# Performance work log

Measured on AMD Instinct MI355X. Metric: run time of the kernel, lower is better.

The kernel has to match this reference:

```python
import jax, jax.numpy as jnp
import numpy as np

B, S, D, E = 4, 2048, 1024, 8
HD = D // E          # per-expert head dim = 128
ROPE = HD // 2       # rotary dims = 64 (32 complex pairs)


def setup_inputs() -> dict:
    key = jax.random.key(0)
    ks = jax.random.split(key, 5)
    x = jax.random.normal(ks[0], (B, S, D), dtype=jnp.float32)
    Wg = jax.random.normal(ks[1], (D, E), dtype=jnp.float32) * 0.02
    Wqkv = jax.random.normal(ks[2], (E, D, 3 * HD), dtype=jnp.float32) * 0.02
    Wff = jax.random.normal(ks[3], (E, HD, D), dtype=jnp.float32) * 0.02
    b_ff = jnp.zeros((D,), dtype=jnp.float32)
    # precompute_freqs_cis(qk_rope_head_dim=ROPE, seqlen=S), theta=10000
    inv = 1.0 / (10000.0 ** (np.arange(0, ROPE, 2, dtype=np.float32) / ROPE))  # [ROPE//2]
    ang = np.arange(S, dtype=np.float32)[:, None] * inv[None, :]               # [S, ROPE//2]
    cos = jnp.asarray(np.cos(ang), dtype=jnp.float32)
    sin = jnp.asarray(np.sin(ang), dtype=jnp.float32)
    return {"x": x, "Wg": Wg, "Wqkv": Wqkv, "Wff": Wff, "b_ff": b_ff, "cos": cos, "sin": sin}


def _apply_rope(x, cos, sin):
    # x: [B,S,E,HD]; rotate the second half (x_pe), keep first half (x_nope), cat (pe, nope)
    b, s, e, hd = x.shape
    x_nope, x_pe = x[..., : hd // 2], x[..., hd // 2 :]
    xr = x_pe.reshape(b, s, e, hd // 4, 2)
    re, im = xr[..., 0], xr[..., 1]
    c = cos[None, :, None, :]
    sn = sin[None, :, None, :]
    rot = jnp.stack([re * c - im * sn, re * sn + im * c], axis=-1).reshape(b, s, e, hd // 2)
    return jnp.concatenate([rot, x_nope], axis=-1)


def reference(x, Wg, Wqkv, Wff, b_ff, cos, sin):
    b, s, d = x.shape
    e, hd = Wqkv.shape[0], Wqkv.shape[2] // 3
    # RoPE on per-expert chunks
    xh = _apply_rope(x.reshape(b, s, e, hd), cos, sin).reshape(b, s, d)
    # SwitchGate: top-1 routing
    probs = jax.nn.softmax(xh @ Wg, axis=-1)            # [b,s,E]
    expert = jnp.argmax(probs, axis=-1)                 # [b,s]
    gate = jnp.max(probs, axis=-1)                      # [b,s]
    # preprocess: per-expert stable gather of routed tokens (capacity = s, padded+masked)
    is_e = expert[None, :, :] == jnp.arange(e)[:, None, None]        # [E,b,s] bool
    order = jnp.argsort(jnp.where(is_e, 0, 1), axis=-1, stable=True)  # [E,b,s] routed-first
    mask_g = jnp.take_along_axis(is_e, order, axis=-1).astype(xh.dtype)  # [E,b,s]
    x_g = jnp.take_along_axis(xh[None], order[..., None], axis=2)    # [E,b,s,d]
    gate_g = jnp.take_along_axis(gate[None], order, axis=2)          # [E,b,s]
    # expert-grouped column-parallel QKV
    qkv = jnp.einsum("ebsd,edf->ebsf", x_g, Wqkv)                    # [E,b,s,3*hd]
    q, k, v = jnp.split(qkv, 3, axis=-1)                             # [E,b,s,hd]
    # grouped sparse attention within each expert's token set
    dot = jnp.einsum("ebqh,ebkh->ebqk", q, k) / jnp.sqrt(jnp.asarray(hd, xh.dtype))
    dot = dot - 1e6 * (1.0 - mask_g[:, :, None, :])
    attn = jax.nn.softmax(dot, axis=-1)
    ctx = jnp.einsum("ebqk,ebkh->ebqh", attn, v)                     # [E,b,s,hd]
    # row-parallel output projection, gate-weighted
    out = jnp.einsum("ebsh,ehd->ebsd", ctx, Wff) + b_ff
    out = out * (gate_g * mask_g)[..., None]
    # scatter_add combine back to [b,s,d]
    outs = jnp.zeros((b, s, d), dtype=xh.dtype)
    outs = outs.at[jnp.arange(b)[None, :, None], order].add(out)
    return outs
```

## Files before the change

### kernel.cpp

```cpp
#include <hip/hip_runtime.h>
#include <math.h>

#define Bn 4
#define Sn 2048
#define Dn 1024
#define En 8
#define HDn 128
#define NG 32
#define MAXT 160
#define MAXN 1024

typedef __attribute__((ext_vector_type(8))) short bf16x8;
typedef __attribute__((ext_vector_type(4))) float f32x4;
typedef unsigned short u16;

__device__ __forceinline__ unsigned bf16_rn(float x) {
  unsigned u = __float_as_uint(x);
  return (u + 0x7fffu + ((u >> 16) & 1u)) >> 16;
}
__device__ __forceinline__ void bsplit(float x, unsigned& hi, unsigned& lo) {
  hi = bf16_rn(x);
  lo = bf16_rn(x - __uint_as_float(hi << 16));
}
__device__ __forceinline__ void gl16(const void* g, void* l) {
  __builtin_amdgcn_global_load_lds(
      (const __attribute__((address_space(1))) void*)g,
      (__attribute__((address_space(3))) void*)l, 16, 0, 0);
}
#define MFMA16(a, b, c) __builtin_amdgcn_mfma_f32_16x16x32_bf16((a), (b), (c), 0, 0, 0)

__global__ __launch_bounds__(256) void k_rope_gate(
    const float* __restrict__ x, const float* __restrict__ Wg,
    const float* __restrict__ cosT, const float* __restrict__ sinT,
    u16* __restrict__ xh_hi, u16* __restrict__ xh_lo,
    int* __restrict__ expertArr, float* __restrict__ gateArr)
{
  int wid = threadIdx.x >> 6, l = threadIdx.x & 63;
  int bs = (blockIdx.x << 2) + wid;
  int s  = bs & (Sn - 1);
  const float* xrow = x + (size_t)bs * Dn;
  int j0 = l << 4;
  int hb = j0 & ~127;
  int jj = j0 & 127;
  float v[16];
  if (jj < 64) {
    const float* pe = xrow + hb + 64 + jj;
    float a[16];
    *(float4*)(a + 0)  = *(const float4*)(pe + 0);
    *(float4*)(a + 4)  = *(const float4*)(pe + 4);
    *(float4*)(a + 8)  = *(const float4*)(pe + 8);
    *(float4*)(a + 12) = *(const float4*)(pe + 12);
    int p0 = jj >> 1;
#pragma unroll
    for (int i = 0; i < 8; ++i) {
      float c  = cosT[s * 32 + p0 + i];
      float sn = sinT[s * 32 + p0 + i];
      v[2 * i]     = a[2 * i] * c - a[2 * i + 1] * sn;
      v[2 * i + 1] = a[2 * i] * sn + a[2 * i + 1] * c;
    }
  } else {
    const float* np = xrow + hb + (jj - 64);
    *(float4*)(v + 0)  = *(const float4*)(np + 0);
    *(float4*)(v + 4)  = *(const float4*)(np + 4);
    *(float4*)(v + 8)  = *(const float4*)(np + 8);
    *(float4*)(v + 12) = *(const float4*)(np + 12);
  }
  u16 hh[16] __attribute__((aligned(16)));
  u16 ll[16] __attribute__((aligned(16)));
#pragma unroll
  for (int i = 0; i < 16; ++i) {
    unsigned h, lo;
    bsplit(v[i], h, lo);
    hh[i] = (u16)h; ll[i] = (u16)lo;
  }
  *(uint4*)(xh_hi + (size_t)bs * Dn + j0)     = *(uint4*)(hh);
  *(uint4*)(xh_hi + (size_t)bs * Dn + j0 + 8) = *(uint4*)(hh + 8);
  *(uint4*)(xh_lo + (size_t)bs * Dn + j0)     = *(uint4*)(ll);
  *(uint4*)(xh_lo + (size_t)bs * Dn + j0 + 8) = *(uint4*)(ll + 8);

  float pl[8] = {0.f, 0.f, 0.f, 0.f, 0.f, 0.f, 0.f, 0.f};
  const float* wr = Wg + (size_t)j0 * En;
#pragma unroll
  for (int i = 0; i < 16; ++i) {
    float4 w0 = *(const float4*)(wr + i * 8);
    float4 w1 = *(const float4*)(wr + i * 8 + 4);
    float xv = v[i];
    pl[0] += xv * w0.x; pl[1] += xv * w0.y; pl[2] += xv * w0.z; pl[3] += xv * w0.w;
    pl[4] += xv * w1.x; pl[5] += xv * w1.y; pl[6] += xv * w1.z; pl[7] += xv * w1.w;
  }
#pragma unroll
  for (int off = 1; off < 64; off <<= 1) {
#pragma unroll
    for (int e = 0; e < 8; ++e) pl[e] += __shfl_xor(pl[e], off, 64);
  }
  float m = pl[0]; int be = 0;
#pragma unroll
  for (int e = 1; e < 8; ++e) if (pl[e] > m) { m = pl[e]; be = e; }
  float ss = 0.f;
#pragma unroll
  for (int e = 0; e < 8; ++e) ss += expf(pl[e] - m);
  if (l == 0) {
    expertArr[bs] = be;
    gateArr[bs] = 1.0f / ss;
  }
}

__global__ __launch_bounds__(256) void k_prep_w(
    const float* __restrict__ W, u16* __restrict__ hiT, u16* __restrict__ loT,
    int Kdim, int Ndim)
{
  int e = blockIdx.z, k0 = blockIdx.x << 6, c0 = blockIdx.y << 6;
  __shared__ float tile[64][65];
  int t = threadIdx.x;
  int r = t >> 4, cc = (t & 15) << 2;
  const float* src = W + ((size_t)e * Kdim + k0) * Ndim + c0;
#pragma unroll
  for (int i = 0; i < 4; ++i) {
    float4 v = *(const float4*)(src + (size_t)(r + i * 16) * Ndim + cc);
    tile[r + i * 16][cc + 0] = v.x; tile[r + i * 16][cc + 1] = v.y;
    tile[r + i * 16][cc + 2] = v.z; tile[r + i * 16][cc + 3] = v.w;
  }
  __syncthreads();
#pragma unroll
  for (int i = 0; i < 4; ++i) {
    int oc = (t >> 4) + i * 16;
    int ok = (t & 15) << 2;
    float v0 = tile[ok + 0][oc], v1 = tile[ok + 1][oc];
    float v2 = tile[ok + 2][oc], v3 = tile[ok + 3][oc];
    unsigned h0,l0,h1,l1,h2,l2,h3,l3;
    bsplit(v0,h0,l0); bsplit(v1,h1,l1); bsplit(v2,h2,l2); bsplit(v3,h3,l3);
    size_t o = ((size_t)e * Ndim + c0 + oc) * Kdim + k0 + ok;
    *(ushort4*)(hiT + o) = make_ushort4((u16)h0,(u16)h1,(u16)h2,(u16)h3);
    *(ushort4*)(loT + o) = make_ushort4((u16)l0,(u16)l1,(u16)l2,(u16)l3);
  }
}

__global__ __launch_bounds__(256) void k_route(
    const int* __restrict__ expertArr, int* __restrict__ idx, int* __restrict__ cnt)
{
  int g = blockIdx.x;
  int b = g >> 3, e = g & 7;
  int t = threadIdx.x;
  __shared__ int wtot[4];
  __shared__ int base;
  if (t == 0) base = 0;
  __syncthreads();
  for (int c = 0; c < Sn; c += 256) {
    int s = c + t;
    int pred = (expertArr[b * Sn + s] == e) ? 1 : 0;
    unsigned long long mask = __ballot(pred);
    int ln = t & 63, wv = t >> 6;
    int wpre = __popcll(mask & ((1ull << ln) - 1ull));
    if (ln == 63) wtot[wv] = wpre + pred;
    __syncthreads();
    int woff = 0;
    for (int w = 0; w < wv; ++w) woff += wtot[w];
    int tot = wtot[0] + wtot[1] + wtot[2] + wtot[3];
    if (pred) idx[(g << 11) + base + woff + wpre] = s;
    __syncthreads();
    if (t == 0) base += tot;
    __syncthreads();
  }
  if (t == 0) cnt[g] = base;
}

__global__ void k_tiles(const int* __restrict__ cnt, int* __restrict__ tileg,
                        int* __restrict__ tilem, int* __restrict__ ntile)
{
  if (threadIdx.x == 0 && blockIdx.x == 0) {
    int t = 0;
    for (int g = 0; g < NG; ++g) {
      int n = cnt[g];
      for (int m0 = 0; m0 < n && t < MAXT; m0 += 64) { tileg[t] = g; tilem[t] = m0; ++t; }
    }
    ntile[0] = t;
  }
}

__global__ __launch_bounds__(256) void k_qkv(
    const u16* __restrict__ xh_hi, const u16* __restrict__ xh_lo,
    const u16* __restrict__ WqT_hi, const u16* __restrict__ WqT_lo,
    const int* __restrict__ idx, const int* __restrict__ cnt,
    const int* __restrict__ tileg, const int* __restrict__ tilem,
    const int* __restrict__ ntile,
    u16* __restrict__ qkv_hi, u16* __restrict__ qkv_lo,
    u16* __restrict__ vT_hi, u16* __restrict__ vT_lo)
{
  extern __shared__ unsigned char LDS[];
  int tid = blockIdx.x;
  if (tid >= ntile[0]) return;
  int g = tileg[tid], m0 = tilem[tid];
  int n = cnt[g];
  int b = g >> 3, e = g & 7;
  const int* idxg = idx + (g << 11);
  int n0 = blockIdx.y << 6;
  int t = threadIdx.x;
  int wid = t >> 6, l = t & 63;
  int wr = wid >> 1, wc = wid & 1;
  int lc = l & 15, lq = l >> 4;

  int srow = t >> 2;
  int sslot = (t & 3) ^ ((srow >> 1) & 3);
  int rgs = m0 + srow; rgs = rgs < n ? rgs : n - 1;
  size_t aoffR = ((size_t)(b * Sn + idxg[rgs])) * Dn + sslot * 8;
  size_t boffR = ((size_t)e * 384 + n0 + srow) * Dn + sslot * 8;
  unsigned dst = (unsigned)t << 4;

  f32x4 acc[2][2];
#pragma unroll
  for (int i = 0; i < 2; ++i)
#pragma unroll
    for (int j = 0; j < 2; ++j) acc[i][j] = (f32x4){0.f, 0.f, 0.f, 0.f};

  int rA0 = wr * 32 + lc, rA1 = rA0 + 16;
  int cB0 = wc * 32 + lc, cB1 = cB0 + 16;
  unsigned swA = (unsigned)((lq ^ ((rA0 >> 1) & 3)) << 4);
  unsigned swB = (unsigned)((lq ^ ((cB0 >> 1) & 3)) << 4);
  unsigned bA0 = rA0 * 64 + swA, bA1 = rA1 * 64 + swA;
  unsigned bB0 = 8192 + cB0 * 64 + swB, bB1 = 8192 + cB1 * 64 + swB;

#define STAGE(bb, k0)                                                \
  do {                                                               \
    gl16(xh_hi + aoffR + (k0), LDS + (bb) + dst);                    \
    gl16(xh_lo + aoffR + (k0), LDS + (bb) + 4096 + dst);             \
    gl16(WqT_hi + boffR + (k0), LDS + (bb) + 8192 + dst);            \
    gl16(WqT_lo + boffR + (k0), LDS + (bb) + 12288 + dst);           \
  } while (0)

  STAGE(0, 0);
  __syncthreads();
  for (int tt = 0; tt < 32; ++tt) {
    unsigned cur = (tt & 1) ? 16384u : 0u;
    if (tt < 31) STAGE(cur ^ 16384u, (tt + 1) * 32);
    bf16x8 ah0 = *(const bf16x8*)(LDS + cur + bA0);
    bf16x8 ah1 = *(const bf16x8*)(LDS + cur + bA1);
    bf16x8 al0 = *(const bf16x8*)(LDS + cur + bA0 + 4096);
    bf16x8 al1 = *(const bf16x8*)(LDS + cur + bA1 + 4096);
    bf16x8 bh0 = *(const bf16x8*)(LDS + cur + bB0);
    bf16x8 bh1 = *(const bf16x8*)(LDS + cur + bB1);
    bf16x8 bl0 = *(const bf16x8*)(LDS + cur + bB0 + 4096);
    bf16x8 bl1 = *(const bf16x8*)(LDS + cur + bB1 + 4096);
    acc[0][0] = MFMA16(ah0, bh0, acc[0][0]);
    acc[0][1] = MFMA16(ah0, bh1, acc[0][1]);
    acc[1][0] = MFMA16(ah1, bh0, acc[1][0]);
    acc[1][1] = MFMA16(ah1, bh1, acc[1][1]);
    acc[0][0] = MFMA16(al0, bh0, acc[0][0]);
    acc[0][1] = MFMA16(al0, bh1, acc[0][1]);
    acc[1][0] = MFMA16(al1, bh0, acc[1][0]);
    acc[1][1] = MFMA16(al1, bh1, acc[1][1]);
    acc[0][0] = MFMA16(ah0, bl0, acc[0][0]);
    acc[0][1] = MFMA16(ah0, bl1, acc[0][1]);
    acc[1][0] = MFMA16(ah1, bl0, acc[1][0]);
    acc[1][1] = MFMA16(ah1, bl1, acc[1][1]);
    __syncthreads();
  }
#undef STAGE

#pragma unroll
  for (int fi = 0; fi < 2; ++fi) {
#pragma unroll
    for (int rr = 0; rr < 4; ++rr) {
      int rg = m0 + wr * 32 + fi * 16 + lq * 4 + rr;
      if (rg < n) {
        int tok = idxg[rg];
#pragma unroll
        for (int fj = 0; fj < 2; ++fj) {
          int col = n0 + wc * 32 + fj * 16 + lc;
          unsigned h, lo2;
          bsplit(acc[fi][fj][rr], h, lo2);
          if (col < 256) {
            size_t o = (size_t)(b * Sn + tok) * 384 + col;
            qkv_hi[o] = (u16)h; qkv_lo[o] = (u16)lo2;
          } else {
            size_t o = ((size_t)g * HDn + (col - 256)) * MAXN + rg;
            vT_hi[o] = (u16)h; vT_lo[o] = (u16)lo2;
          }
        }
      }
    }
  }
}

__global__ __launch_bounds__(256) void k_attn(
    const u16* __restrict__ qkv_hi, const u16* __restrict__ qkv_lo,
    const u16* __restrict__ vT_hi, const u16* __restrict__ vT_lo,
    const int* __restrict__ idx, const int* __restrict__ cnt,
    const int* __restrict__ tileg, const int* __restrict__ tilem,
    const int* __restrict__ ntile,
    u16* __restrict__ ctx_hi, u16* __restrict__ ctx_lo)
{
  extern __shared__ unsigned char LDS[];
  int tid = blockIdx.x;
  if (tid >= ntile[0]) return;
  int g = tileg[tid], m0 = tilem[tid];
  int n = cnt[g];
  int b = g >> 3;
  const int* idxg = idx + (g << 11);
  int t = threadIdx.x, wid = t >> 6, l = t & 63;
  int lc = l & 15, lq = l >> 4;
  const float scale = 0.08838834764831845f;

  int qrg = m0 + wid * 16 + lc; qrg = qrg < n ? qrg : n - 1;
  size_t qoff = (size_t)(b * Sn + idxg[qrg]) * 384 + lq * 8;
  bf16x8 Qhi[4], Qlo[4];
#pragma unroll
  for (int ks = 0; ks < 4; ++ks) {
    Qhi[ks] = *(const bf16x8*)(qkv_hi + qoff + ks * 32);
    Qlo[ks] = *(const bf16x8*)(qkv_lo + qoff + ks * 32);
  }

  f32x4 acc[8];
#pragma unroll
  for (int i = 0; i < 8; ++i) acc[i] = (f32x4){0.f, 0.f, 0.f, 0.f};
  float m_r[4] = {-1e30f, -1e30f, -1e30f, -1e30f};
  float l_r[4] = {0.f, 0.f, 0.f, 0.f};

  size_t vbase = ((size_t)g * HDn + lc) * MAXN + lq * 8;
  unsigned pbase = 65536u + wid * 4096u;

#define STAGEK(bufb, kc)                                                     \
  do {                                                                       \
    unsigned bb = (bufb);                                                    \
    for (int j = 0; j < 4; ++j) {                                            \
      int c = wid * 4 + j;                                                   \
      int row = (kc) + c * 4 + lq;                                           \
      int rg = row < n ? row : n - 1;                                        \
      int srcslot = lc ^ (((c & 1) << 2) | lq);                              \
      size_t soff = (size_t)(b * Sn + idxg[rg]) * 384 + 128 + srcslot * 8;   \
      gl16(qkv_hi + soff, LDS + bb + c * 1024);                              \
      gl16(qkv_lo + soff, LDS + bb + 16384 + c * 1024);                      \
    }                                                                        \
  } while (0)

  int nt = (n + 63) >> 6;
  STAGEK(0, 0);
  __syncthreads();

  for (int tt = 0; tt < nt; ++tt) {
    unsigned cur = (tt & 1) ? 32768u : 0u;
    if (tt + 1 < nt) STAGEK(cur ^ 32768u, (tt + 1) * 64);
    int kc = tt * 64;

    f32x4 Sf[4];
#pragma unroll
    for (int kf = 0; kf < 4; ++kf) Sf[kf] = (f32x4){0.f, 0.f, 0.f, 0.f};
#pragma unroll
    for (int ks = 0; ks < 4; ++ks) {
#pragma unroll
      for (int kf = 0; kf < 4; ++kf) {
        int row = kf * 16 + lc;
        unsigned byte = cur + row * 256 + ((((ks << 2) | lq) ^ (row & 7)) << 4);
        bf16x8 kh = *(const bf16x8*)(LDS + byte);
        bf16x8 kl = *(const bf16x8*)(LDS + byte + 16384);
        Sf[kf] = MFMA16(Qhi[ks], kh, Sf[kf]);
        Sf[kf] = MFMA16(Qlo[ks], kh, Sf[kf]);
        Sf[kf] = MFMA16(Qhi[ks], kl, Sf[kf]);
      }
    }

    float mloc[4] = {-1e30f, -1e30f, -1e30f, -1e30f};
#pragma unroll
    for (int kf = 0; kf < 4; ++kf) {
#pragma unroll
      for (int r = 0; r < 4; ++r) {
        int key = kc + kf * 16 + lc;
        float s = (key < n) ? Sf[kf][r] * scale : -1e30f;
        Sf[kf][r] = s;
        mloc[r] = fmaxf(mloc[r], s);
      }
    }
#pragma unroll
    for (int off = 1; off < 16; off <<= 1) {
#pragma unroll
      for (int r = 0; r < 4; ++r) mloc[r] = fmaxf(mloc[r], __shfl_xor(mloc[r], off, 64));
    }
    float corr[4], rs[4] = {0.f, 0.f, 0.f, 0.f};
#pragma unroll
    for (int r = 0; r < 4; ++r) {
      float mn = fmaxf(m_r[r], mloc[r]);
      corr[r] = expf(m_r[r] - mn);
      m_r[r] = mn;
    }
#pragma unroll
    for (int kf = 0; kf < 4; ++kf) {
#pragma unroll
      for (int r = 0; r < 4; ++r) {
        float p = expf(Sf[kf][r] - m_r[r]);
        rs[r] += p;
        unsigned ph, plo;
        bsplit(p, ph, plo);
        int prow = (lq << 2) | r;
        int slot = (kf << 1) | (lc >> 3);
        unsigned pb = pbase + prow * 128 + ((slot ^ (prow & 7)) << 4) + ((lc & 7) << 1);
        *(u16*)(LDS + pb) = (u16)ph;
        *(u16*)(LDS + pb + 2048) = (u16)plo;
      }
    }
#pragma unroll
    for (int off = 1; off < 16; off <<= 1) {
#pragma unroll
      for (int r = 0; r < 4; ++r) rs[r] += __shfl_xor(rs[r], off, 64);
    }
#pragma unroll
    for (int r = 0; r < 4; ++r) l_r[r] = l_r[r] * corr[r] + rs[r];
#pragma unroll
    for (int df = 0; df < 8; ++df)
#pragma unroll
      for (int r = 0; r < 4; ++r) acc[df][r] *= corr[r];

#pragma unroll
    for (int ks2 = 0; ks2 < 2; ++ks2) {
      unsigned pr = pbase + lc * 128 + ((((ks2 << 2) | lq) ^ (lc & 7)) << 4);
      bf16x8 pa = *(const bf16x8*)(LDS + pr);
      bf16x8 pl = *(const bf16x8*)(LDS + pr + 2048);
#pragma unroll
      for (int df = 0; df < 8; ++df) {
        size_t vo = vbase + (size_t)(df * 16) * MAXN + kc + ks2 * 32;
        bf16x8 vh = *(const bf16x8*)(vT_hi + vo);
        bf16x8 vl = *(const bf16x8*)(vT_lo + vo);
        acc[df] = MFMA16(pa, vh, acc[df]);
        acc[df] = MFMA16(pl, vh, acc[df]);
        acc[df] = MFMA16(pa, vl, acc[df]);
      }
    }
    __syncthreads();
  }
#undef STAGEK

#pragma unroll
  for (int r = 0; r < 4; ++r) {
    int rg = m0 + wid * 16 + (lq << 2) + r;
    if (rg < n) {
      int tok = idxg[rg];
      float inv = 1.0f / l_r[r];
      size_t o = (size_t)(b * Sn + tok) * HDn + lc;
#pragma unroll
      for (int df = 0; df < 8; ++df) {
        unsigned h, lo2;
        bsplit(acc[df][r] * inv, h, lo2);
        ctx_hi[o + df * 16] = (u16)h;
        ctx_lo[o + df * 16] = (u16)lo2;
      }
    }
  }
}

__global__ __launch_bounds__(256) void k_out(
    const u16* __restrict__ ctx_hi, const u16* __restrict__ ctx_lo,
    const u16* __restrict__ WfT_hi, const u16* __restrict__ WfT_lo,
    const float* __restrict__ bff,
    const int* __restrict__ idx, const int* __restrict__ cnt,
    const int* __restrict__ tileg, const int* __restrict__ tilem,
    const int* __restrict__ ntile,
    const float* __restrict__ gateArr,
    float* __restrict__ out)
{
  int tid = blockIdx.x;
  if (tid >= ntile[0]) return;
  int g = tileg[tid], m0 = tilem[tid];
  int n = cnt[g];
  int b = g >> 3, e = g & 7;
  const int* idxg = idx + (g << 11);
  int t = threadIdx.x, wid = t >> 6, l = t & 63;
  int lc = l & 15, lq = l >> 4;
  int n0 = blockIdx.y * 256 + wid * 64;

  f32x4 acc[4][4];
#pragma unroll
  for (int i = 0; i < 4; ++i)
#pragma unroll
    for (int j = 0; j < 4; ++j) acc[i][j] = (f32x4){0.f, 0.f, 0.f, 0.f};

  size_t aoff[4];
#pragma unroll
  for (int fi = 0; fi < 4; ++fi) {
    int rg = m0 + fi * 16 + lc; rg = rg < n ? rg : n - 1;
    aoff[fi] = ((size_t)(b * Sn + idxg[rg])) * HDn + lq * 8;
  }
  size_t boff[4];
#pragma unroll
  for (int fj = 0; fj < 4; ++fj)
    boff[fj] = ((size_t)e * Dn + n0 + fj * 16 + lc) * HDn + lq * 8;

#pragma unroll
  for (int ks = 0; ks < 4; ++ks) {
    int ko = ks * 32;
    bf16x8 ah[4], al[4], bh[4], bl[4];
#pragma unroll
    for (int fi = 0; fi < 4; ++fi) {
      ah[fi] = *(const bf16x8*)(ctx_hi + aoff[fi] + ko);
      al[fi] = *(const bf16x8*)(ctx_lo + aoff[fi] + ko);
    }
#pragma unroll
    for (int fj = 0; fj < 4; ++fj) {
      bh[fj] = *(const bf16x8*)(WfT_hi + boff[fj] + ko);
      bl[fj] = *(const bf16x8*)(WfT_lo + boff[fj] + ko);
    }
#pragma unroll
    for (int fi = 0; fi < 4; ++fi)
#pragma unroll
      for (int fj = 0; fj < 4; ++fj) {
        acc[fi][fj] = MFMA16(ah[fi], bh[fj], acc[fi][fj]);
        acc[fi][fj] = MFMA16(al[fi], bh[fj], acc[fi][fj]);
        acc[fi][fj] = MFMA16(ah[fi], bl[fj], acc[fi][fj]);
      }
  }

  float bv[4];
#pragma unroll
  for (int fj = 0; fj < 4; ++fj) bv[fj] = bff[n0 + fj * 16 + lc];

#pragma unroll
  for (int fi = 0; fi < 4; ++fi) {
#pragma unroll
    for (int rr = 0; rr < 4; ++rr) {
      int rg = m0 + fi * 16 + lq * 4 + rr;
      if (rg < n) {
        int tok = idxg[rg];
        float gt = gateArr[b * Sn + tok];
        float* orow = out + ((size_t)(b * Sn + tok)) * Dn + n0 + lc;
#pragma unroll
        for (int fj = 0; fj < 4; ++fj)
          orow[fj * 16] = (acc[fi][fj][rr] + bv[fj]) * gt;
      }
    }
  }
}

extern "C" void kernel_launch(void* const* d_in, const int* in_sizes, int n_in,
                              void* d_out, int out_size, void* d_ws, size_t ws_size,
                              hipStream_t stream) {
  const float* x    = (const float*)d_in[0];
  const float* Wg   = (const float*)d_in[1];
  const float* Wqkv = (const float*)d_in[2];
  const float* Wff  = (const float*)d_in[3];
  const float* bff  = (const float*)d_in[4];
  const float* cosT = (const float*)d_in[5];
  const float* sinT = (const float*)d_in[6];
  float* out = (float*)d_out;

  size_t off = 0;
  auto carve = [&](size_t bytes) -> void* {
    void* p = (char*)d_ws + off;
    off += (bytes + 255) & ~(size_t)255;
    return p;
  };
  u16* xh_hi  = (u16*)carve((size_t)Bn * Sn * Dn * 2);
  u16* xh_lo  = (u16*)carve((size_t)Bn * Sn * Dn * 2);
  u16* WqT_hi = (u16*)carve((size_t)En * 384 * Dn * 2);
  u16* WqT_lo = (u16*)carve((size_t)En * 384 * Dn * 2);
  u16* WfT_hi = (u16*)carve((size_t)En * Dn * HDn * 2);
  u16* WfT_lo = (u16*)carve((size_t)En * Dn * HDn * 2);
  u16* qkv_hi = (u16*)carve((size_t)Bn * Sn * 384 * 2);
  u16* qkv_lo = (u16*)carve((size_t)Bn * Sn * 384 * 2);
  u16* vT_hi  = (u16*)carve((size_t)NG * HDn * MAXN * 2);
  u16* vT_lo  = (u16*)carve((size_t)NG * HDn * MAXN * 2);
  u16* ctx_hi = (u16*)carve((size_t)Bn * Sn * HDn * 2);
  u16* ctx_lo = (u16*)carve((size_t)Bn * Sn * HDn * 2);
  float* gateArr = (float*)carve((size_t)Bn * Sn * sizeof(float));
  int*   expertA = (int*)carve((size_t)Bn * Sn * sizeof(int));
  int*   idx     = (int*)carve((size_t)NG * Sn * sizeof(int));
  int*   cnt     = (int*)carve((size_t)NG * sizeof(int));
  int*   tileg   = (int*)carve((size_t)MAXT * sizeof(int));
  int*   tilem   = (int*)carve((size_t)MAXT * sizeof(int));
  int*   ntile   = (int*)carve(256);
  (void)ws_size; (void)in_sizes; (void)n_in; (void)out_size;

  hipFuncSetAttribute((const void*)k_attn, hipFuncAttributeMaxDynamicSharedMemorySize, 81920);

  k_rope_gate<<<dim3(Bn * Sn / 4), dim3(256), 0, stream>>>(x, Wg, cosT, sinT, xh_hi, xh_lo, expertA, gateArr);
  k_prep_w<<<dim3(16, 6, 8), dim3(256), 0, stream>>>(Wqkv, WqT_hi, WqT_lo, Dn, 384);
  k_prep_w<<<dim3(2, 16, 8), dim3(256), 0, stream>>>(Wff, WfT_hi, WfT_lo, HDn, Dn);
  k_route<<<dim3(NG), dim3(256), 0, stream>>>(expertA, idx, cnt);
  k_tiles<<<dim3(1), dim3(64), 0, stream>>>(cnt, tileg, tilem, ntile);
  k_qkv<<<dim3(MAXT, 6), dim3(256), 32768, stream>>>(xh_hi, xh_lo, WqT_hi, WqT_lo, idx, cnt, tileg, tilem, ntile, qkv_hi, qkv_lo, vT_hi, vT_lo);
  k_attn<<<dim3(MAXT), dim3(256), 81920, stream>>>(qkv_hi, qkv_lo, vT_hi, vT_lo, idx, cnt, tileg, tilem, ntile, ctx_hi, ctx_lo);
  k_out<<<dim3(MAXT, 4), dim3(256), 0, stream>>>(ctx_hi, ctx_lo, WfT_hi, WfT_lo, bff, idx, cnt, tileg, tilem, ntile, gateArr, out);
}
```

Measured before the change: 195.3 us.

## Widen QKV GEMM tiles to 64x192 with a static per-group block mapping

The QKV projection kernel now has each block compute a 64x192 output tile instead of 64x64. Each wave owns 48 columns across all 64 rows, so the gathered activation rows are staged twice per token instead of six times. The data-dependent tile list (tileg/tilem/ntile) is replaced by a fixed 384-block grid: each block derives its group, row tile and column half from its block index and exits early if the row tile is past that group's token count. In exchange the kernel doubles LDS use to 64KB and holds more accumulators, which lowers occupancy. The fixed grid also covers at most 384 tokens per (batch, expert) group.

```diff
diff --git a/kernel.cpp b/kernel.cpp
--- a/kernel.cpp
+++ b/kernel.cpp
@@ -181,91 +181,91 @@
     const u16* __restrict__ xh_hi, const u16* __restrict__ xh_lo,
     const u16* __restrict__ WqT_hi, const u16* __restrict__ WqT_lo,
     const int* __restrict__ idx, const int* __restrict__ cnt,
-    const int* __restrict__ tileg, const int* __restrict__ tilem,
-    const int* __restrict__ ntile,
     u16* __restrict__ qkv_hi, u16* __restrict__ qkv_lo,
     u16* __restrict__ vT_hi, u16* __restrict__ vT_lo)
 {
   extern __shared__ unsigned char LDS[];
-  int tid = blockIdx.x;
-  if (tid >= ntile[0]) return;
-  int g = tileg[tid], m0 = tilem[tid];
+  int bid = blockIdx.x;
+  int r8 = bid & 7, q = bid >> 3;
+  int g = r8 + ((q & 3) << 3);
+  int slot = q >> 2;
+  int m0 = (slot >> 1) << 6;
+  int n0 = (slot & 1) * 192;
   int n = cnt[g];
+  if (m0 >= n) return;
   int b = g >> 3, e = g & 7;
   const int* idxg = idx + (g << 11);
-  int n0 = blockIdx.y << 6;
   int t = threadIdx.x;
-  int wid = t >> 6, l = t & 63;
-  int wr = wid >> 1, wc = wid & 1;
+  int w = t >> 6, l = t & 63;
   int lc = l & 15, lq = l >> 4;
 
   int srow = t >> 2;
   int sslot = (t & 3) ^ ((srow >> 1) & 3);
   int rgs = m0 + srow; rgs = rgs < n ? rgs : n - 1;
   size_t aoffR = ((size_t)(b * Sn + idxg[rgs])) * Dn + sslot * 8;
-  size_t boffR = ((size_t)e * 384 + n0 + srow) * Dn + sslot * 8;
+  size_t boffR0 = ((size_t)e * 384 + n0 + srow) * Dn + sslot * 8;
   unsigned dst = (unsigned)t << 4;
 
-  f32x4 acc[2][2];
-#pragma unroll
-  for (int i = 0; i < 2; ++i)
-#pragma unroll
-    for (int j = 0; j < 2; ++j) acc[i][j] = (f32x4){0.f, 0.f, 0.f, 0.f};
-
-  int rA0 = wr * 32 + lc, rA1 = rA0 + 16;
-  int cB0 = wc * 32 + lc, cB1 = cB0 + 16;
-  unsigned swA = (unsigned)((lq ^ ((rA0 >> 1) & 3)) << 4);
-  unsigned swB = (unsigned)((lq ^ ((cB0 >> 1) & 3)) << 4);
-  unsigned bA0 = rA0 * 64 + swA, bA1 = rA1 * 64 + swA;
-  unsigned bB0 = 8192 + cB0 * 64 + swB, bB1 = 8192 + cB1 * 64 + swB;
-
-#define STAGE(bb, k0)                                                \
-  do {                                                               \
-    gl16(xh_hi + aoffR + (k0), LDS + (bb) + dst);                    \
-    gl16(xh_lo + aoffR + (k0), LDS + (bb) + 4096 + dst);             \
-    gl16(WqT_hi + boffR + (k0), LDS + (bb) + 8192 + dst);            \
-    gl16(WqT_lo + boffR + (k0), LDS + (bb) + 12288 + dst);           \
+  f32x4 acc[4][3];
+#pragma unroll
+  for (int i = 0; i < 4; ++i)
+#pragma unroll
+    for (int j = 0; j < 3; ++j) acc[i][j] = (f32x4){0.f, 0.f, 0.f, 0.f};
+
+  unsigned off = (unsigned)((lq ^ ((lc >> 1) & 3)) << 4);
+
+#define STAGE(bb, k0)                                                 \
+  do {                                                                \
+    gl16(xh_hi + aoffR + (k0), LDS + (bb) + dst);                     \
+    gl16(xh_lo + aoffR + (k0), LDS + (bb) + 4096 + dst);              \
+    gl16(WqT_hi + boffR0 + (k0), LDS + (bb) + 8192 + dst);            \
+    gl16(WqT_hi + boffR0 + (size_t)64 * Dn + (k0), LDS + (bb) + 12288 + dst); \
+    gl16(WqT_hi + boffR0 + (size_t)128 * Dn + (k0), LDS + (bb) + 16384 + dst);\
+    gl16(WqT_lo + boffR0 + (k0), LDS + (bb) + 20480 + dst);           \
+    gl16(WqT_lo + boffR0 + (size_t)64 * Dn + (k0), LDS + (bb) + 24576 + dst); \
+    gl16(WqT_lo + boffR0 + (size_t)128 * Dn + (k0), LDS + (bb) + 28672 + dst);\
   } while (0)
 
   STAGE(0, 0);
   __syncthreads();
   for (int tt = 0; tt < 32; ++tt) {
-    unsigned cur = (tt & 1) ? 16384u : 0u;
-    if (tt < 31) STAGE(cur ^ 16384u, (tt + 1) * 32);
-    bf16x8 ah0 = *(const bf16x8*)(LDS + cur + bA0);
-    bf16x8 ah1 = *(const bf16x8*)(LDS + cur + bA1);
-    bf16x8 al0 = *(const bf16x8*)(LDS + cur + bA0 + 4096);
-    bf16x8 al1 = *(const bf16x8*)(LDS + cur + bA1 + 4096);
-    bf16x8 bh0 = *(const bf16x8*)(LDS + cur + bB0);
-    bf16x8 bh1 = *(const bf16x8*)(LDS + cur + bB1);
-    bf16x8 bl0 = *(const bf16x8*)(LDS + cur + bB0 + 4096);
-    bf16x8 bl1 = *(const bf16x8*)(LDS + cur + bB1 + 4096);
-    acc[0][0] = MFMA16(ah0, bh0, acc[0][0]);
-    acc[0][1] = MFMA16(ah0, bh1, acc[0][1]);
-    acc[1][0] = MFMA16(ah1, bh0, acc[1][0]);
-    acc[1][1] = MFMA16(ah1, bh1, acc[1][1]);
-    acc[0][0] = MFMA16(al0, bh0, acc[0][0]);
-    acc[0][1] = MFMA16(al0, bh1, acc[0][1]);
-    acc[1][0] = MFMA16(al1, bh0, acc[1][0]);
-    acc[1][1] = MFMA16(al1, bh1, acc[1][1]);
-    acc[0][0] = MFMA16(ah0, bl0, acc[0][0]);
-    acc[0][1] = MFMA16(ah0, bl1, acc[0][1]);
-    acc[1][0] = MFMA16(ah1, bl0, acc[1][0]);
-    acc[1][1] = MFMA16(ah1, bl1, acc[1][1]);
+    unsigned cur = (tt & 1) ? 32768u : 0u;
+    if (tt < 31) STAGE(cur ^ 32768u, (tt + 1) * 32);
+    bf16x8 ah[4], al[4], bh[3], bl[3];
+#pragma unroll
+    for (int fi = 0; fi < 4; ++fi) {
+      unsigned ab = cur + (unsigned)((fi * 16 + lc) * 64) + off;
+      ah[fi] = *(const bf16x8*)(LDS + ab);
+      al[fi] = *(const bf16x8*)(LDS + ab + 4096);
+    }
+#pragma unroll
+    for (int fj = 0; fj < 3; ++fj) {
+      unsigned bb2 = cur + 8192u + (unsigned)((w * 48 + fj * 16 + lc) * 64) + off;
+      bh[fj] = *(const bf16x8*)(LDS + bb2);
+      bl[fj] = *(const bf16x8*)(LDS + bb2 + 12288);
+    }
+#pragma unroll
+    for (int fi = 0; fi < 4; ++fi)
+#pragma unroll
+      for (int fj = 0; fj < 3; ++fj) {
+        acc[fi][fj] = MFMA16(ah[fi], bh[fj], acc[fi][fj]);
+        acc[fi][fj] = MFMA16(al[fi], bh[fj], acc[fi][fj]);
+        acc[fi][fj] = MFMA16(ah[fi], bl[fj], acc[fi][fj]);
+      }
     __syncthreads();
   }
 #undef STAGE
 
 #pragma unroll
-  for (int fi = 0; fi < 2; ++fi) {
+  for (int fi = 0; fi < 4; ++fi) {
 #pragma unroll
     for (int rr = 0; rr < 4; ++rr) {
-      int rg = m0 + wr * 32 + fi * 16 + lq * 4 + rr;
+      int rg = m0 + fi * 16 + lq * 4 + rr;
       if (rg < n) {
         int tok = idxg[rg];
 #pragma unroll
-        for (int fj = 0; fj < 2; ++fj) {
-          int col = n0 + wc * 32 + fj * 16 + lc;
+        for (int fj = 0; fj < 3; ++fj) {
+          int col = n0 + w * 48 + fj * 16 + lc;
           unsigned h, lo2;
           bsplit(acc[fi][fj][rr], h, lo2);
           if (col < 256) {
@@ -573,7 +573,7 @@
   k_prep_w<<<dim3(2, 16, 8), dim3(256), 0, stream>>>(Wff, WfT_hi, WfT_lo, HDn, Dn);
   k_route<<<dim3(NG), dim3(256), 0, stream>>>(expertA, idx, cnt);
   k_tiles<<<dim3(1), dim3(64), 0, stream>>>(cnt, tileg, tilem, ntile);
-  k_qkv<<<dim3(MAXT, 6), dim3(256), 32768, stream>>>(xh_hi, xh_lo, WqT_hi, WqT_lo, idx, cnt, tileg, tilem, ntile, qkv_hi, qkv_lo, vT_hi, vT_lo);
+  k_qkv<<<dim3(384), dim3(256), 65536, stream>>>(xh_hi, xh_lo, WqT_hi, WqT_lo, idx, cnt, qkv_hi, qkv_lo, vT_hi, vT_lo);
   k_attn<<<dim3(MAXT), dim3(256), 81920, stream>>>(qkv_hi, qkv_lo, vT_hi, vT_lo, idx, cnt, tileg, tilem, ntile, ctx_hi, ctx_lo);
   k_out<<<dim3(MAXT, 4), dim3(256), 0, stream>>>(ctx_hi, ctx_lo, WfT_hi, WfT_lo, bff, idx, cnt, tileg, tilem, ntile, gateArr, out);
 }
```

Measured after the change: 191.2 us. 1.02x faster.
